# Performance work log

Measured on AMD Instinct MI355X. Metric: run time of the kernel, lower is better.

The kernel has to match this reference:

```python
import jax, jax.numpy as jnp
import numpy as np

B, T, D = 4, 4096, 1024
C = 8.0  # RG_LRU constant c
LOGIT_LO = float(np.log(0.9 / 0.1))    # logit(0.9)
LOGIT_HI = float(np.log(0.999 / 0.001))  # logit(0.999)


def setup_inputs() -> dict:
    key = jax.random.key(0)
    ks = jax.random.split(key, 12)
    s = 1.0 / np.sqrt(D)
    z = lambda: jnp.zeros((D,), jnp.float32)
    return {
        "x": jax.random.normal(ks[0], (B, T, D), jnp.float32),
        "g1": jnp.ones((D,), jnp.float32),
        "g2": jnp.ones((D,), jnp.float32),
        # RecurrentBlock: shared linear, kernel-1 conv, output linear
        "W_lin": jax.random.normal(ks[1], (D, D), jnp.float32) * s, "b_lin": z(),
        "W_conv": jax.random.normal(ks[2], (D, D), jnp.float32) * s, "b_conv": z(),
        "W_lin2": jax.random.normal(ks[3], (D, D), jnp.float32) * s, "b_lin2": z(),
        # RG_LRU params
        "Wa": jax.random.normal(ks[4], (D, D), jnp.float32) * s, "ba": z(),
        "Wx": jax.random.normal(ks[5], (D, D), jnp.float32) * s, "bx": z(),
        "Lam": jax.random.uniform(ks[6], (D,), jnp.float32, LOGIT_LO, LOGIT_HI),
        # GatedMLPBlock
        "W1": jax.random.normal(ks[7], (D, D), jnp.float32) * s, "b1": z(),
        "W2": jax.random.normal(ks[8], (D, D), jnp.float32) * s, "b2": z(),
        "W3": jax.random.normal(ks[9], (D, D), jnp.float32) * s, "b3": z(),
    }


def rms_norm(x, g):
    # F.normalize(x, dim=-1) * sqrt(d) * g
    n = jnp.maximum(jnp.linalg.norm(x, axis=-1, keepdims=True), 1e-12)
    return (x / n) * (x.shape[-1] ** 0.5) * g


def rg_lru(x, Wa, ba, Wx, bx, Lam):
    # x: [B, T, D]
    rt = jax.nn.sigmoid(jnp.einsum('btd,hd->bth', x, Wa) + ba)
    it = jax.nn.sigmoid(jnp.einsum('btd,hd->bth', x, Wx) + bx)
    log_a = -jax.nn.softplus(-Lam)          # [D]
    a = jnp.exp(log_a * rt / C)             # [B, T, D]
    gated = jnp.sqrt(1.0 - a * a) * (it * x)

    def step(h, ag):
        at, gt = ag
        h = at * h + gt
        return h, h

    h0 = jnp.zeros((x.shape[0], x.shape[2]), x.dtype)
    _, hs = jax.lax.scan(step, h0, (jnp.swapaxes(a, 0, 1), jnp.swapaxes(gated, 0, 1)))
    return jnp.swapaxes(hs, 0, 1)           # [B, T, D]


def reference(x, g1, g2, W_lin, b_lin, W_conv, b_conv, W_lin2, b_lin2,
              Wa, ba, Wx, bx, Lam, W1, b1, W2, b2, W3, b3):
    residual = x
    xn = rms_norm(x, g1)

    # RecurrentBlock (note: same linear used for both branches, as in source)
    lin = xn @ W_lin.T + b_lin
    x_gel = jax.nn.gelu(lin, approximate=False)
    x_rg = lin @ W_conv.T + b_conv          # Conv1d kernel_size=1 == pointwise linear
    x_rg = rg_lru(x_rg, Wa, ba, Wx, bx, Lam)
    xr = (x_gel * x_rg) @ W_lin2.T + b_lin2

    residual = xr + residual
    xm = rms_norm(residual, g2)

    # GatedMLPBlock
    out = jax.nn.sigmoid(xm @ W1.T + b1)
    gate = jax.nn.gelu(out, approximate=False)
    combined = gate * (xm @ W2.T + b2)
    y = combined @ W3.T + b3
    return y + residual
```

## Files before the change

kernel.cpp:

```cpp
#include <hip/hip_runtime.h>
#include <cstdint>
#include <cstddef>

typedef unsigned short u16;
typedef __attribute__((ext_vector_type(8))) __bf16 bf16x8;
typedef __attribute__((ext_vector_type(4))) float f32x4;

#define DD 1024
#define MM 16384
#define NCH 64
#define CLEN 64
#define EPAD2 264
#define EPADF 260

__device__ __forceinline__ u16 f2b(float f) {
    uint32_t u = __float_as_uint(f);
    u += 0x7fffu + ((u >> 16) & 1u);
    return (u16)(u >> 16);
}
__device__ __forceinline__ float b2f(u16 v) {
    return __uint_as_float(((uint32_t)v) << 16);
}
__device__ __forceinline__ float sigmoid_f(float v) { return 1.f / (1.f + __expf(-v)); }
__device__ __forceinline__ float gelu_f(float v) {
    return 0.5f * v * (1.f + erff(v * 0.70710678118654752f));
}

__device__ __forceinline__ void glds16(const u16* g, u16* l) {
    __builtin_amdgcn_global_load_lds(
        (const __attribute__((address_space(1))) void*)g,
        (__attribute__((address_space(3))) void*)l, 16, 0, 0);
}

__device__ __forceinline__ void swiz8(int l, int& mt, int& nt) {
    mt = (l & 7) * 8 + ((l >> 3) & 7);
    nt = l >> 6;
}

#define ACC(i, j) ((i) < 4 ? accL[(i) & 3][(j)] : accH[(i) & 3][(j)])

template <int MODE>
__global__ __launch_bounds__(512, 2)
void gemm256(const u16* __restrict__ A, const u16* __restrict__ Bw,
             const float* __restrict__ bias, const float* __restrict__ biasB,
             const float* __restrict__ auxf,
             u16* __restrict__ outb, float* __restrict__ outf)
{
    __shared__ __align__(16) u16 smem[65536];

    int mt, nt; swiz8(blockIdx.x, mt, nt);
    const int m0 = mt * 256, n0 = nt * 256;
    const int tid = threadIdx.x;
    const int wave = tid >> 6, lane = tid & 63;
    const int wm = (wave >> 2) * 128, wn = (wave & 3) * 64;
    const int lr = lane & 15, lq = lane >> 4;

    const int trow = tid >> 2, tcol = tid & 3;
    const int kswz = (tcol ^ ((trow >> 1) & 3)) * 8;
    const u16* Ag = A + (size_t)(m0 + trow) * DD + kswz;
    const u16* Bg = Bw + (size_t)(n0 + trow) * DD + kswz;
    const int st = tid * 8;
    const int cs = (lq ^ ((lr >> 1) & 3)) * 8;

    f32x4 accL[4][4] = {}, accH[4][4] = {};
    bf16x8 av[4], bv[4];

    auto SA = [&](int kt) {
        u16* Ls = smem + (kt & 3) * 16384;
        const u16* a = Ag + (size_t)kt * 32;
        glds16(a, Ls + st);
        glds16(a + (size_t)128 * DD, Ls + 4096 + st);
    };
    auto SB = [&](int kt) {
        u16* Ls = smem + (kt & 3) * 16384 + 8192;
        const u16* b = Bg + (size_t)kt * 32;
        glds16(b, Ls + st);
        glds16(b + (size_t)64 * DD + (size_t)64 * DD, Ls + 4096 + st);
    };
    auto RDA = [&](int kt, int rb) {
        const u16* Ls = smem + (kt & 3) * 16384;
#pragma unroll
        for (int i = 0; i < 4; i++)
            av[i] = *(const bf16x8*)&Ls[(rb + i * 16 + lr) * 32 + cs];
    };
    auto RDB = [&](int kt) {
        const u16* Ls = smem + (kt & 3) * 16384 + 8192;
#pragma unroll
        for (int j = 0; j < 4; j++)
            bv[j] = *(const bf16x8*)&Ls[(wn + j * 16 + lr) * 32 + cs];
    };
    auto MM16 = [&](f32x4 (&ac)[4][4]) {
        __builtin_amdgcn_s_setprio(1);
#pragma unroll
        for (int i = 0; i < 4; i++)
#pragma unroll
            for (int j = 0; j < 4; j++)
                ac[i][j] = __builtin_amdgcn_mfma_f32_16x16x32_bf16(
                    av[i], bv[j], ac[i][j], 0, 0, 0);
        __builtin_amdgcn_s_setprio(0);
    };

    SA(0); SB(0); SA(1); SB(1); SA(2); SB(2);
    asm volatile("s_waitcnt vmcnt(8)\ns_barrier" ::: "memory");

#pragma unroll 4
    for (int kt = 0; kt < 29; ++kt) {
        RDA(kt, wm); RDB(kt);
        SA(kt + 3);
        asm volatile("s_barrier" ::: "memory");
        MM16(accL);
        asm volatile("s_barrier" ::: "memory");
        RDA(kt, wm + 64);
        SB(kt + 3);
        asm volatile("s_waitcnt vmcnt(8)\ns_barrier" ::: "memory");
        MM16(accH);
        asm volatile("s_barrier" ::: "memory");
    }
    RDA(29, wm); RDB(29);
    asm volatile("s_barrier" ::: "memory");
    MM16(accL);
    asm volatile("s_barrier" ::: "memory");
    RDA(29, wm + 64);
    asm volatile("s_waitcnt vmcnt(4)\ns_barrier" ::: "memory");
    MM16(accH);
    asm volatile("s_barrier" ::: "memory");
    RDA(30, wm); RDB(30);
    asm volatile("s_barrier" ::: "memory");
    MM16(accL);
    asm volatile("s_barrier" ::: "memory");
    RDA(30, wm + 64);
    asm volatile("s_waitcnt vmcnt(0)\ns_barrier" ::: "memory");
    MM16(accH);
    asm volatile("s_barrier" ::: "memory");
    RDA(31, wm); RDB(31);
    MM16(accL);
    RDA(31, wm + 64);
    MM16(accH);

    if constexpr (MODE == 0 || MODE == 1) {
        const int NW = (MODE == 1) ? 2048 : 1024;
        u16* ep = smem;
#pragma unroll
        for (int h = 0; h < 4; ++h) {
            __syncthreads();
            if (wm == (h >> 1) * 128) {
                const int i0 = (h & 1) * 4;
#pragma unroll
                for (int ii = 0; ii < 4; ++ii) {
#pragma unroll
                    for (int j = 0; j < 4; ++j) {
                        const int col = wn + j * 16 + lr;
                        const int gc = n0 + col;
                        float bz;
                        if constexpr (MODE == 1)
                            bz = (gc & 1) ? biasB[gc >> 1] : bias[gc >> 1];
                        else
                            bz = bias[gc];
#pragma unroll
                        for (int p = 0; p < 4; ++p) {
                            float v = ACC(i0 + ii, j)[p] + bz;
                            if constexpr (MODE == 1) v = sigmoid_f(v);
                            ep[(ii * 16 + lq * 4 + p) * EPAD2 + col] = f2b(v);
                        }
                    }
                }
            }
            __syncthreads();
#pragma unroll
            for (int t = 0; t < 4; ++t) {
                const int f = t * 512 + tid;
                const int row = f >> 5, c8 = (f & 31) * 8;
                *(uint4*)&outb[(size_t)(m0 + h * 64 + row) * NW + n0 + c8] =
                    *(const uint4*)&ep[row * EPAD2 + c8];
            }
        }
    } else if constexpr (MODE == 2) {
#pragma unroll
        for (int i = 0; i < 8; ++i) {
            const int mrow = m0 + wm + (i & 3) * 16 + (i >> 2) * 64 + lq * 4;
#pragma unroll
            for (int j = 0; j < 4; ++j) {
                const int ncol = n0 + wn + j * 16 + lr;
                const float bz = bias[ncol];
#pragma unroll
                for (int p = 0; p < 4; ++p) {
                    const size_t idx = (size_t)(mrow + p) * DD + ncol;
                    outf[idx] = ((i < 4) ? accL[i & 3][j][p] : accH[i & 3][j][p])
                                + bz + auxf[idx];
                }
            }
        }
    } else {
        float* epf = (float*)smem;
#pragma unroll
        for (int h = 0; h < 4; ++h) {
            __syncthreads();
            if (wm == (h >> 1) * 128) {
                const int i0 = (h & 1) * 4;
#pragma unroll
                for (int ii = 0; ii < 4; ++ii) {
#pragma unroll
                    for (int j = 0; j < 4; ++j) {
                        const int col = wn + j * 16 + lr;
                        const int gc = n0 + col;
                        const float bz = (gc & 1) ? biasB[gc >> 1] : bias[gc >> 1];
#pragma unroll
                        for (int p = 0; p < 4; ++p)
                            epf[(ii * 16 + lq * 4 + p) * EPADF + col] =
                                ACC(i0 + ii, j)[p] + bz;
                    }
                }
            }
            __syncthreads();
#pragma unroll
            for (int t = 0; t < 4; ++t) {
                const int f = t * 512 + tid;
                const int row = f >> 5, cg = (f & 31) * 4;
                const float4 v0 = *(const float4*)&epf[row * EPADF + cg * 2];
                const float4 v1 = *(const float4*)&epf[row * EPADF + cg * 2 + 4];
                ushort4 o4;
                o4.x = f2b(gelu_f(sigmoid_f(v0.x)) * v0.y);
                o4.y = f2b(gelu_f(sigmoid_f(v0.z)) * v0.w);
                o4.z = f2b(gelu_f(sigmoid_f(v1.x)) * v1.y);
                o4.w = f2b(gelu_f(sigmoid_f(v1.z)) * v1.w);
                *(ushort4*)&outb[(size_t)(m0 + h * 64 + row) * DD + (n0 >> 1) + cg] = o4;
            }
        }
    }
}

__global__ __launch_bounds__(256)
void rmsnorm_k(const float* __restrict__ x, const float* __restrict__ g,
               u16* __restrict__ out)
{
    const int row = blockIdx.x;
    const int t = threadIdx.x;
    const float4 v = ((const float4*)(x + (size_t)row * DD))[t];
    float ss = v.x * v.x + v.y * v.y + v.z * v.z + v.w * v.w;
#pragma unroll
    for (int o = 32; o > 0; o >>= 1) ss += __shfl_down(ss, o, 64);
    __shared__ float wsum[4];
    if ((t & 63) == 0) wsum[t >> 6] = ss;
    __syncthreads();
    const float tot = wsum[0] + wsum[1] + wsum[2] + wsum[3];
    const float sc = 32.0f * rsqrtf(fmaxf(tot, 1e-24f));
    const float4 gv = ((const float4*)g)[t];
    ushort4 o4;
    o4.x = f2b(v.x * sc * gv.x);
    o4.y = f2b(v.y * sc * gv.y);
    o4.z = f2b(v.z * sc * gv.z);
    o4.w = f2b(v.w * sc * gv.w);
    ((ushort4*)(out + (size_t)row * DD))[t] = o4;
}

struct WP { const float* s[4]; unsigned off[4]; };
__global__ __launch_bounds__(256)
void conv_plain(WP w, u16* __restrict__ out)
{
    const float* in = w.s[blockIdx.y];
    u16* o = out + (size_t)w.off[blockIdx.y];
    const int i = (blockIdx.x * 256 + threadIdx.x) * 4;
    const float4 v = *(const float4*)(in + i);
    ushort4 r;
    r.x = f2b(v.x); r.y = f2b(v.y); r.z = f2b(v.z); r.w = f2b(v.w);
    *(ushort4*)(o + i) = r;
}
struct WI { const float* a[2]; const float* b[2]; unsigned off[2]; };
__global__ __launch_bounds__(256)
void conv_inter(WI w, u16* __restrict__ out)
{
    u16* o = out + (size_t)w.off[blockIdx.y];
    const int e = (blockIdx.x * 256 + threadIdx.x) * 4;
    const int row = e >> 10, col = e & 1023;
    const float* src = (row & 1) ? w.b[blockIdx.y] : w.a[blockIdx.y];
    const float4 v = *(const float4*)(src + ((size_t)(row >> 1) << 10) + col);
    ushort4 r;
    r.x = f2b(v.x); r.y = f2b(v.y); r.z = f2b(v.z); r.w = f2b(v.w);
    *(ushort4*)(o + e) = r;
}

__global__ __launch_bounds__(256)
void scan_chunks(const u16* __restrict__ rtit, const u16* __restrict__ rg,
                 const float* __restrict__ Lam,
                 float* __restrict__ P, float* __restrict__ Hl)
{
    const int d = blockIdx.x * 256 + threadIdx.x;
    const int c = blockIdx.y, b = blockIdx.z;
    const float k = -log1pf(__expf(-Lam[d])) * 0.125f;
    const size_t base1 = (((size_t)b * 4096) + (size_t)c * CLEN) * DD + d;
    const size_t base2 = (((size_t)b * 4096) + (size_t)c * CLEN) * 2048 + 2 * d;
    float p = 1.f, h = 0.f;
#pragma unroll 4
    for (int t = 0; t < CLEN; t++) {
        const uint32_t w = *(const uint32_t*)&rtit[base2 + (size_t)t * 2048];
        const float r = b2f((u16)(w & 0xffffu));
        const float i = b2f((u16)(w >> 16));
        const float xv = b2f(rg[base1 + (size_t)t * DD]);
        const float a = __expf(k * r);
        const float g = sqrtf(fmaxf(1.f - a * a, 0.f)) * (i * xv);
        p *= a;
        h = fmaf(a, h, g);
    }
    const int o = (b * NCH + c) * DD + d;
    P[o] = p;
    Hl[o] = h;
}

__global__ __launch_bounds__(256)
void scan_carry(const float* __restrict__ P, const float* __restrict__ Hl,
                float* __restrict__ Cin)
{
    const int idx = blockIdx.x * 256 + threadIdx.x;
    const int b = idx >> 10, d = idx & 1023;
    float h = 0.f;
    for (int c = 0; c < NCH; c++) {
        const int o = (b * NCH + c) * DD + d;
        Cin[o] = h;
        h = fmaf(P[o], h, Hl[o]);
    }
}

__global__ __launch_bounds__(256)
void scan_apply(const u16* __restrict__ rtit, const u16* __restrict__ rg,
                const u16* __restrict__ lin, const float* __restrict__ Lam,
                const float* __restrict__ Cin, u16* __restrict__ yin)
{
    const int d = blockIdx.x * 256 + threadIdx.x;
    const int c = blockIdx.y, b = blockIdx.z;
    const float k = -log1pf(__expf(-Lam[d])) * 0.125f;
    const size_t base1 = (((size_t)b * 4096) + (size_t)c * CLEN) * DD + d;
    const size_t base2 = (((size_t)b * 4096) + (size_t)c * CLEN) * 2048 + 2 * d;
    float h = Cin[(b * NCH + c) * DD + d];
#pragma unroll 4
    for (int t = 0; t < CLEN; t++) {
        const uint32_t w = *(const uint32_t*)&rtit[base2 + (size_t)t * 2048];
        const float r = b2f((u16)(w & 0xffffu));
        const float i = b2f((u16)(w >> 16));
        const size_t ix = base1 + (size_t)t * DD;
        const float xv = b2f(rg[ix]);
        const float a = __expf(k * r);
        const float g = sqrtf(fmaxf(1.f - a * a, 0.f)) * (i * xv);
        h = fmaf(a, h, g);
        const float l = b2f(lin[ix]);
        yin[ix] = f2b(gelu_f(l) * h);
    }
}

extern "C" void kernel_launch(void* const* d_in, const int* in_sizes, int n_in,
                              void* d_out, int out_size, void* d_ws, size_t ws_size,
                              hipStream_t stream)
{
    const float* x      = (const float*)d_in[0];
    const float* g1     = (const float*)d_in[1];
    const float* g2     = (const float*)d_in[2];
    const float* W_lin  = (const float*)d_in[3];
    const float* b_lin  = (const float*)d_in[4];
    const float* W_conv = (const float*)d_in[5];
    const float* b_conv = (const float*)d_in[6];
    const float* W_lin2 = (const float*)d_in[7];
    const float* b_lin2 = (const float*)d_in[8];
    const float* Wa     = (const float*)d_in[9];
    const float* ba     = (const float*)d_in[10];
    const float* Wx     = (const float*)d_in[11];
    const float* bx     = (const float*)d_in[12];
    const float* Lam    = (const float*)d_in[13];
    const float* W1     = (const float*)d_in[14];
    const float* b1     = (const float*)d_in[15];
    const float* W2     = (const float*)d_in[16];
    const float* b2     = (const float*)d_in[17];
    const float* W3     = (const float*)d_in[18];
    const float* b3     = (const float*)d_in[19];
    float* out = (float*)d_out;

    char* p = (char*)d_ws;
    auto alloc = [&](size_t bytes) -> char* {
        char* q = p;
        p += (bytes + 255) & ~(size_t)255;
        return q;
    };
    const size_t MD = (size_t)MM * DD;
    const size_t M1 = (size_t)DD * DD;
    u16* wball = (u16*)alloc((size_t)8 * M1 * 2);
    u16* t1   = (u16*)alloc(MD * 2);
    u16* t2   = (u16*)alloc(MD * 2);
    u16* t4   = (u16*)alloc(MD * 2);
    u16* rtit = (u16*)alloc(MD * 4);
    float* res2 = (float*)alloc(MD * 4);
    float* P   = (float*)alloc((size_t)4 * NCH * DD * 4);
    float* Hl  = (float*)alloc((size_t)4 * NCH * DD * 4);
    float* Cin = (float*)alloc((size_t)4 * NCH * DD * 4);

    WP wp;
    wp.s[0] = W_lin;  wp.off[0] = 0;
    wp.s[1] = W_conv; wp.off[1] = 1u << 20;
    wp.s[2] = W_lin2; wp.off[2] = 4u << 20;
    wp.s[3] = W3;     wp.off[3] = 7u << 20;
    conv_plain<<<dim3(M1 / 1024, 4), 256, 0, stream>>>(wp, wball);
    WI wi;
    wi.a[0] = Wa; wi.b[0] = Wx; wi.off[0] = 2u << 20;
    wi.a[1] = W1; wi.b[1] = W2; wi.off[1] = 5u << 20;
    conv_inter<<<dim3(2 * M1 / 1024, 2), 256, 0, stream>>>(wi, wball);

    const u16* wLin  = wball;
    const u16* wConv = wball + (1u << 20);
    const u16* wAX   = wball + (2u << 20);
    const u16* wLin2 = wball + (4u << 20);
    const u16* w12   = wball + (5u << 20);
    const u16* w3    = wball + (7u << 20);

    const int gs = (MM / 256) * (DD / 256);
    const int gw = (MM / 256) * (2 * DD / 256);
    const dim3 sg(DD / 256, NCH, 4);

    rmsnorm_k<<<MM, 256, 0, stream>>>(x, g1, t4);
    gemm256<0><<<gs, 512, 0, stream>>>(t4, wLin, b_lin, nullptr, nullptr, t1, nullptr);
    gemm256<0><<<gs, 512, 0, stream>>>(t1, wConv, b_conv, nullptr, nullptr, t2, nullptr);
    gemm256<1><<<gw, 512, 0, stream>>>(t2, wAX, ba, bx, nullptr, rtit, nullptr);
    scan_chunks<<<sg, 256, 0, stream>>>(rtit, t2, Lam, P, Hl);
    scan_carry<<<4096 / 256, 256, 0, stream>>>(P, Hl, Cin);
    scan_apply<<<sg, 256, 0, stream>>>(rtit, t2, t1, Lam, Cin, t4);
    gemm256<2><<<gs, 512, 0, stream>>>(t4, wLin2, b_lin2, nullptr, x, nullptr, res2);
    rmsnorm_k<<<MM, 256, 0, stream>>>(res2, g2, t4);
    gemm256<3><<<gw, 512, 0, stream>>>(t4, w12, b1, b2, nullptr, t2, nullptr);
    gemm256<2><<<gs, 512, 0, stream>>>(t2, w3, b3, nullptr, res2, nullptr, out);
}
```

Baseline: 605.8 us.

## Use 128x128 tile GEMM kernel for square N=1024 projections

Adds a 256-thread 128x128-tile double-buffered GEMM kernel and routes the four DxD projections (linear, conv, lin2 with residual, W3 with residual) to it, keeping the 256x256 kernel only for the fused N=2048 gate GEMMs. With 256x256 tiles the square GEMMs launch only 256 blocks, which leaves CUs underfilled at 2 blocks per CU. The smaller tile gives 1024 blocks and better occupancy, at the cost of lower operand reuse per tile and a simpler, less pipelined K loop.

```diff
diff --git a/kernel.cpp b/kernel.cpp
--- a/kernel.cpp
+++ b/kernel.cpp
@@ -10,6 +10,7 @@
 #define MM 16384
 #define NCH 64
 #define CLEN 64
+#define EPAD 136
 #define EPAD2 264
 #define EPADF 260
 
@@ -32,9 +33,124 @@
         (__attribute__((address_space(3))) void*)l, 16, 0, 0);
 }
 
+__device__ __forceinline__ void swiz(int l, int& mt, int& nt) {
+    const int g = l >> 6, r = l & 63;
+    mt = g * 8 + (r & 7);
+    nt = r >> 3;
+}
 __device__ __forceinline__ void swiz8(int l, int& mt, int& nt) {
     mt = (l & 7) * 8 + ((l >> 3) & 7);
     nt = l >> 6;
+}
+
+template <int MODE>
+__global__ __launch_bounds__(256, 3)
+void gemm_bt(const u16* __restrict__ A, const u16* __restrict__ Bw,
+             const float* __restrict__ bias, const float* __restrict__ auxf,
+             u16* __restrict__ outb, float* __restrict__ outf)
+{
+    const int K = DD, N = DD;
+    __shared__ __align__(16) u16 smem[16384];
+    u16* const As0 = smem;
+    u16* const Bs0 = smem + 4096;
+    u16* const As1 = smem + 8192;
+    u16* const Bs1 = smem + 12288;
+
+    int mt, nt; swiz(blockIdx.x, mt, nt);
+    const int m0 = mt * 128, n0 = nt * 128;
+    const int tid = threadIdx.x;
+    const int wave = tid >> 6, lane = tid & 63;
+    const int wm = (wave >> 1) * 64, wn = (wave & 1) * 64;
+    const int lr = lane & 15, lq = lane >> 4;
+
+    const int trow = tid >> 2, tcol = tid & 3;
+    const int kswz = (tcol ^ ((trow >> 1) & 3)) * 8;
+    const u16* Ag = A + (size_t)(m0 + trow) * K + kswz;
+    const u16* Bg = Bw + (size_t)(n0 + trow) * K + kswz;
+    const int st = tid * 8;
+    const int cs = (lq ^ ((lr >> 1) & 3)) * 8;
+
+    f32x4 acc[4][4] = {};
+
+    glds16(Ag, As0 + st);
+    glds16(Ag + (size_t)64 * K, As0 + st + 2048);
+    glds16(Bg, Bs0 + st);
+    glds16(Bg + (size_t)64 * K, Bs0 + st + 2048);
+
+#pragma unroll 2
+    for (int k0 = 0; k0 < K; k0 += 32) {
+        u16* const Ac = ((k0 >> 5) & 1) ? As1 : As0;
+        u16* const Bc = ((k0 >> 5) & 1) ? Bs1 : Bs0;
+        if (k0 + 32 < K) {
+            u16* const An = ((k0 >> 5) & 1) ? As0 : As1;
+            u16* const Bn = ((k0 >> 5) & 1) ? Bs0 : Bs1;
+            const int kn = k0 + 32;
+            glds16(Ag + kn, An + st);
+            glds16(Ag + (size_t)64 * K + kn, An + st + 2048);
+            glds16(Bg + kn, Bn + st);
+            glds16(Bg + (size_t)64 * K + kn, Bn + st + 2048);
+            asm volatile("s_waitcnt vmcnt(4)\ns_barrier" ::: "memory");
+        } else {
+            asm volatile("s_waitcnt vmcnt(0)\ns_barrier" ::: "memory");
+        }
+
+        bf16x8 av[4], bv[4];
+#pragma unroll
+        for (int i = 0; i < 4; i++)
+            av[i] = *(const bf16x8*)&Ac[(wm + i * 16 + lr) * 32 + cs];
+#pragma unroll
+        for (int j = 0; j < 4; j++)
+            bv[j] = *(const bf16x8*)&Bc[(wn + j * 16 + lr) * 32 + cs];
+#pragma unroll
+        for (int i = 0; i < 4; i++)
+#pragma unroll
+            for (int j = 0; j < 4; j++)
+                acc[i][j] = __builtin_amdgcn_mfma_f32_16x16x32_bf16(
+                    av[i], bv[j], acc[i][j], 0, 0, 0);
+        asm volatile("s_barrier" ::: "memory");
+    }
+
+    if constexpr (MODE == 0) {
+        for (int half = 0; half < 2; half++) {
+            __syncthreads();
+            if (wm == half * 64) {
+#pragma unroll
+                for (int i = 0; i < 4; i++)
+#pragma unroll
+                    for (int j = 0; j < 4; j++) {
+                        const int col = wn + j * 16 + lr;
+                        const float bz = bias[n0 + col];
+#pragma unroll
+                        for (int p = 0; p < 4; p++)
+                            smem[(i * 16 + lq * 4 + p) * EPAD + col] =
+                                f2b(acc[i][j][p] + bz);
+                    }
+            }
+            __syncthreads();
+#pragma unroll
+            for (int t = 0; t < 4; t++) {
+                const int f = t * 256 + tid;
+                const int row = f >> 4, c8 = (f & 15) * 8;
+                *(uint4*)&outb[(size_t)(m0 + half * 64 + row) * N + n0 + c8] =
+                    *(const uint4*)&smem[row * EPAD + c8];
+            }
+        }
+    } else {
+#pragma unroll
+        for (int i = 0; i < 4; i++) {
+            const int mrow = m0 + wm + i * 16 + lq * 4;
+#pragma unroll
+            for (int j = 0; j < 4; j++) {
+                const int ncol = n0 + wn + j * 16 + lr;
+                const float bz = bias[ncol];
+#pragma unroll
+                for (int p = 0; p < 4; p++) {
+                    const size_t idx = (size_t)(mrow + p) * N + ncol;
+                    outf[idx] = acc[i][j][p] + bz + auxf[idx];
+                }
+            }
+        }
+    }
 }
 
 #define ACC(i, j) ((i) < 4 ? accL[(i) & 3][(j)] : accH[(i) & 3][(j)])
@@ -43,8 +159,7 @@
 __global__ __launch_bounds__(512, 2)
 void gemm256(const u16* __restrict__ A, const u16* __restrict__ Bw,
              const float* __restrict__ bias, const float* __restrict__ biasB,
-             const float* __restrict__ auxf,
-             u16* __restrict__ outb, float* __restrict__ outf)
+             u16* __restrict__ outb)
 {
     __shared__ __align__(16) u16 smem[65536];
 
@@ -75,7 +190,7 @@
         u16* Ls = smem + (kt & 3) * 16384 + 8192;
         const u16* b = Bg + (size_t)kt * 32;
         glds16(b, Ls + st);
-        glds16(b + (size_t)64 * DD + (size_t)64 * DD, Ls + 4096 + st);
+        glds16(b + (size_t)128 * DD, Ls + 4096 + st);
     };
     auto RDA = [&](int kt, int rb) {
         const u16* Ls = smem + (kt & 3) * 16384;
@@ -137,8 +252,7 @@
     RDA(31, wm + 64);
     MM16(accH);
 
-    if constexpr (MODE == 0 || MODE == 1) {
-        const int NW = (MODE == 1) ? 2048 : 1024;
+    if constexpr (MODE == 1) {
         u16* ep = smem;
 #pragma unroll
         for (int h = 0; h < 4; ++h) {
@@ -151,17 +265,11 @@
                     for (int j = 0; j < 4; ++j) {
                         const int col = wn + j * 16 + lr;
                         const int gc = n0 + col;
-                        float bz;
-                        if constexpr (MODE == 1)
-                            bz = (gc & 1) ? biasB[gc >> 1] : bias[gc >> 1];
-                        else
-                            bz = bias[gc];
-#pragma unroll
-                        for (int p = 0; p < 4; ++p) {
-                            float v = ACC(i0 + ii, j)[p] + bz;
-                            if constexpr (MODE == 1) v = sigmoid_f(v);
-                            ep[(ii * 16 + lq * 4 + p) * EPAD2 + col] = f2b(v);
-                        }
+                        const float bz = (gc & 1) ? biasB[gc >> 1] : bias[gc >> 1];
+#pragma unroll
+                        for (int p = 0; p < 4; ++p)
+                            ep[(ii * 16 + lq * 4 + p) * EPAD2 + col] =
+                                f2b(sigmoid_f(ACC(i0 + ii, j)[p] + bz));
                     }
                 }
             }
@@ -170,24 +278,8 @@
             for (int t = 0; t < 4; ++t) {
                 const int f = t * 512 + tid;
                 const int row = f >> 5, c8 = (f & 31) * 8;
-                *(uint4*)&outb[(size_t)(m0 + h * 64 + row) * NW + n0 + c8] =
+                *(uint4*)&outb[(size_t)(m0 + h * 64 + row) * 2048 + n0 + c8] =
                     *(const uint4*)&ep[row * EPAD2 + c8];
-            }
-        }
-    } else if constexpr (MODE == 2) {
-#pragma unroll
-        for (int i = 0; i < 8; ++i) {
-            const int mrow = m0 + wm + (i & 3) * 16 + (i >> 2) * 64 + lq * 4;
-#pragma unroll
-            for (int j = 0; j < 4; ++j) {
-                const int ncol = n0 + wn + j * 16 + lr;
-                const float bz = bias[ncol];
-#pragma unroll
-                for (int p = 0; p < 4; ++p) {
-                    const size_t idx = (size_t)(mrow + p) * DD + ncol;
-                    outf[idx] = ((i < 4) ? accL[i & 3][j][p] : accH[i & 3][j][p])
-                                + bz + auxf[idx];
-                }
             }
         }
     } else {
@@ -408,19 +500,19 @@
     const u16* w12   = wball + (5u << 20);
     const u16* w3    = wball + (7u << 20);
 
-    const int gs = (MM / 256) * (DD / 256);
+    const int gg = (MM / 128) * (DD / 128);
     const int gw = (MM / 256) * (2 * DD / 256);
     const dim3 sg(DD / 256, NCH, 4);
 
     rmsnorm_k<<<MM, 256, 0, stream>>>(x, g1, t4);
-    gemm256<0><<<gs, 512, 0, stream>>>(t4, wLin, b_lin, nullptr, nullptr, t1, nullptr);
-    gemm256<0><<<gs, 512, 0, stream>>>(t1, wConv, b_conv, nullptr, nullptr, t2, nullptr);
-    gemm256<1><<<gw, 512, 0, stream>>>(t2, wAX, ba, bx, nullptr, rtit, nullptr);
+    gemm_bt<0><<<gg, 256, 0, stream>>>(t4, wLin, b_lin, nullptr, t1, nullptr);
+    gemm_bt<0><<<gg, 256, 0, stream>>>(t1, wConv, b_conv, nullptr, t2, nullptr);
+    gemm256<1><<<gw, 512, 0, stream>>>(t2, wAX, ba, bx, rtit);
     scan_chunks<<<sg, 256, 0, stream>>>(rtit, t2, Lam, P, Hl);
     scan_carry<<<4096 / 256, 256, 0, stream>>>(P, Hl, Cin);
     scan_apply<<<sg, 256, 0, stream>>>(rtit, t2, t1, Lam, Cin, t4);
-    gemm256<2><<<gs, 512, 0, stream>>>(t4, wLin2, b_lin2, nullptr, x, nullptr, res2);
+    gemm_bt<2><<<gg, 256, 0, stream>>>(t4, wLin2, b_lin2, x, nullptr, res2);
     rmsnorm_k<<<MM, 256, 0, stream>>>(res2, g2, t4);
-    gemm256<3><<<gw, 512, 0, stream>>>(t4, w12, b1, b2, nullptr, t2, nullptr);
-    gemm256<2><<<gs, 512, 0, stream>>>(t2, w3, b3, nullptr, res2, nullptr, out);
-}
+    gemm256<3><<<gw, 512, 0, stream>>>(t4, w12, b1, b2, t2);
+    gemm_bt<2><<<gg, 256, 0, stream>>>(t2, w3, b3, res2, nullptr, out);
+}
```

Result: slower. 623.4 us (+2.9%).

## Restructure GEMM main loop to K=64 double-buffered tiles with 8-phase schedule

Applied to the files above, without the earlier changes.

Changes the shared GEMM kernel from a 4-stage ring of K=32 tiles to a 2-buffer scheme with K=64 tiles. Global-to-LDS loads are split into half-tile pieces and interleaved across eight MFMA phases per iteration, with a new XOR swizzle sized for 64-wide rows. The aim is to halve loop iterations and barrier overhead per unit of K and to overlap loads with compute more evenly. In exchange, prefetch depth drops to two buffers, which may expose memory latency, and the finer barrier schedule adds synchronization points.

```diff
diff --git a/kernel.cpp b/kernel.cpp
--- a/kernel.cpp
+++ b/kernel.cpp
@@ -38,13 +38,15 @@
 }
 
 #define ACC(i, j) ((i) < 4 ? accL[(i) & 3][(j)] : accH[(i) & 3][(j)])
+#define MFMA16x32(a, b, c) __builtin_amdgcn_mfma_f32_16x16x32_bf16(a, b, c, 0, 0, 0)
+#define BAR asm volatile("s_barrier" ::: "memory")
 
 template <int MODE>
 __global__ __launch_bounds__(512, 2)
-void gemm256(const u16* __restrict__ A, const u16* __restrict__ Bw,
-             const float* __restrict__ bias, const float* __restrict__ biasB,
-             const float* __restrict__ auxf,
-             u16* __restrict__ outb, float* __restrict__ outf)
+void gemm8p(const u16* __restrict__ A, const u16* __restrict__ Bw,
+            const float* __restrict__ bias, const float* __restrict__ biasB,
+            const float* __restrict__ auxf,
+            u16* __restrict__ outb, float* __restrict__ outf)
 {
     __shared__ __align__(16) u16 smem[65536];
 
@@ -55,90 +57,122 @@
     const int wm = (wave >> 2) * 128, wn = (wave & 3) * 64;
     const int lr = lane & 15, lq = lane >> 4;
 
-    const int trow = tid >> 2, tcol = tid & 3;
-    const int kswz = (tcol ^ ((trow >> 1) & 3)) * 8;
-    const u16* Ag = A + (size_t)(m0 + trow) * DD + kswz;
-    const u16* Bg = Bw + (size_t)(n0 + trow) * DD + kswz;
+    const int kswz = ((tid & 7) ^ ((tid >> 3) & 7)) * 8;
+    const u16* Ag = A + (size_t)(m0 + (tid >> 3)) * DD + kswz;
+    const u16* Bg = Bw + (size_t)(n0 + (tid >> 3)) * DD + kswz;
     const int st = tid * 8;
-    const int cs = (lq ^ ((lr >> 1) & 3)) * 8;
+
+    const int cs0 = ((lq ^ (lr & 7))) * 8;
+    const int cs1 = cs0 ^ 32;
+    const int aLo = (wm + lr) * 64;
+    const int bB  = (wn + lr) * 64;
 
     f32x4 accL[4][4] = {}, accH[4][4] = {};
-    bf16x8 av[4], bv[4];
-
-    auto SA = [&](int kt) {
-        u16* Ls = smem + (kt & 3) * 16384;
-        const u16* a = Ag + (size_t)kt * 32;
-        glds16(a, Ls + st);
-        glds16(a + (size_t)128 * DD, Ls + 4096 + st);
-    };
-    auto SB = [&](int kt) {
-        u16* Ls = smem + (kt & 3) * 16384 + 8192;
-        const u16* b = Bg + (size_t)kt * 32;
-        glds16(b, Ls + st);
-        glds16(b + (size_t)64 * DD + (size_t)64 * DD, Ls + 4096 + st);
-    };
-    auto RDA = [&](int kt, int rb) {
-        const u16* Ls = smem + (kt & 3) * 16384;
-#pragma unroll
-        for (int i = 0; i < 4; i++)
-            av[i] = *(const bf16x8*)&Ls[(rb + i * 16 + lr) * 32 + cs];
-    };
-    auto RDB = [&](int kt) {
-        const u16* Ls = smem + (kt & 3) * 16384 + 8192;
-#pragma unroll
-        for (int j = 0; j < 4; j++)
-            bv[j] = *(const bf16x8*)&Ls[(wn + j * 16 + lr) * 32 + cs];
-    };
-    auto MM16 = [&](f32x4 (&ac)[4][4]) {
+    bf16x8 a_lo[4][2], a_hi[4][2], b_lo[2][2], b_hi[2][2];
+
+    auto STA = [&](int kt, int h, int bb) {
+        u16* Ls = smem + bb * 32768 + h * 8192 + st;
+        const u16* g = Ag + (size_t)(h * 128) * DD + kt * 64;
+        glds16(g, Ls);
+        glds16(g + (size_t)64 * DD, Ls + 4096);
+    };
+    auto STB = [&](int kt, int h, int bb) {
+        u16* Ls = smem + bb * 32768 + 16384 + h * 8192 + st;
+        const u16* g = Bg + (size_t)(h * 128) * DD + kt * 64;
+        glds16(g, Ls);
+        glds16(g + (size_t)64 * DD, Ls + 4096);
+    };
+    auto RDA4 = [&](bf16x8 (&a)[4][2], int base) {
+#pragma unroll
+        for (int i = 0; i < 4; i++) {
+            a[i][0] = *(const bf16x8*)&smem[base + i * 1024 + cs0];
+            a[i][1] = *(const bf16x8*)&smem[base + i * 1024 + cs1];
+        }
+    };
+    auto RDB2 = [&](bf16x8 (&b)[2][2], int base) {
+#pragma unroll
+        for (int j = 0; j < 2; j++) {
+            b[j][0] = *(const bf16x8*)&smem[base + j * 1024 + cs0];
+            b[j][1] = *(const bf16x8*)&smem[base + j * 1024 + cs1];
+        }
+    };
+    auto MM_jL = [&](bf16x8 (&a)[4][2], f32x4 (&ac)[4][4]) {
         __builtin_amdgcn_s_setprio(1);
 #pragma unroll
-        for (int i = 0; i < 4; i++)
-#pragma unroll
-            for (int j = 0; j < 4; j++)
-                ac[i][j] = __builtin_amdgcn_mfma_f32_16x16x32_bf16(
-                    av[i], bv[j], ac[i][j], 0, 0, 0);
+        for (int i = 0; i < 4; i++) {
+            ac[i][0] = MFMA16x32(a[i][0], b_lo[0][0], ac[i][0]);
+            ac[i][0] = MFMA16x32(a[i][1], b_lo[0][1], ac[i][0]);
+            ac[i][1] = MFMA16x32(a[i][0], b_lo[1][0], ac[i][1]);
+            ac[i][1] = MFMA16x32(a[i][1], b_lo[1][1], ac[i][1]);
+        }
         __builtin_amdgcn_s_setprio(0);
     };
-
-    SA(0); SB(0); SA(1); SB(1); SA(2); SB(2);
-    asm volatile("s_waitcnt vmcnt(8)\ns_barrier" ::: "memory");
-
-#pragma unroll 4
-    for (int kt = 0; kt < 29; ++kt) {
-        RDA(kt, wm); RDB(kt);
-        SA(kt + 3);
-        asm volatile("s_barrier" ::: "memory");
-        MM16(accL);
-        asm volatile("s_barrier" ::: "memory");
-        RDA(kt, wm + 64);
-        SB(kt + 3);
-        asm volatile("s_waitcnt vmcnt(8)\ns_barrier" ::: "memory");
-        MM16(accH);
-        asm volatile("s_barrier" ::: "memory");
-    }
-    RDA(29, wm); RDB(29);
-    asm volatile("s_barrier" ::: "memory");
-    MM16(accL);
-    asm volatile("s_barrier" ::: "memory");
-    RDA(29, wm + 64);
-    asm volatile("s_waitcnt vmcnt(4)\ns_barrier" ::: "memory");
-    MM16(accH);
-    asm volatile("s_barrier" ::: "memory");
-    RDA(30, wm); RDB(30);
-    asm volatile("s_barrier" ::: "memory");
-    MM16(accL);
-    asm volatile("s_barrier" ::: "memory");
-    RDA(30, wm + 64);
-    asm volatile("s_waitcnt vmcnt(0)\ns_barrier" ::: "memory");
-    MM16(accH);
-    asm volatile("s_barrier" ::: "memory");
-    RDA(31, wm); RDB(31);
-    MM16(accL);
-    RDA(31, wm + 64);
-    MM16(accH);
+    auto MM_jH = [&](bf16x8 (&a)[4][2], f32x4 (&ac)[4][4]) {
+        __builtin_amdgcn_s_setprio(1);
+#pragma unroll
+        for (int i = 0; i < 4; i++) {
+            ac[i][2] = MFMA16x32(a[i][0], b_hi[0][0], ac[i][2]);
+            ac[i][2] = MFMA16x32(a[i][1], b_hi[0][1], ac[i][2]);
+            ac[i][3] = MFMA16x32(a[i][0], b_hi[1][0], ac[i][3]);
+            ac[i][3] = MFMA16x32(a[i][1], b_hi[1][1], ac[i][3]);
+        }
+        __builtin_amdgcn_s_setprio(0);
+    };
+
+    STA(0, 0, 0); STA(0, 1, 0); STB(0, 0, 0); STB(0, 1, 0);
+    STB(1, 0, 1); STB(1, 1, 1); STA(1, 0, 1);
+    asm volatile("s_waitcnt vmcnt(6)\ns_barrier" ::: "memory");
+
+#pragma unroll 2
+    for (int kt = 0; kt < 14; ++kt) {
+        const int db = kt & 1, nb = db ^ 1;
+        const int dbo = db * 32768;
+        RDA4(a_lo, dbo + aLo);
+        RDB2(b_lo, dbo + 16384 + bB);
+        STA(kt + 1, 1, nb);
+        BAR;
+        MM_jL(a_lo, accL);
+        BAR;
+        RDB2(b_hi, dbo + 16384 + bB + 2048);
+        BAR;
+        MM_jH(a_lo, accL);
+        BAR;
+        RDA4(a_hi, dbo + aLo + 4096);
+        STB(kt + 2, 0, db);
+        BAR;
+        MM_jH(a_hi, accH);
+        BAR;
+        STB(kt + 2, 1, db);
+        STA(kt + 2, 0, db);
+        BAR;
+        MM_jL(a_hi, accH);
+        asm volatile("s_waitcnt vmcnt(6)\ns_barrier" ::: "memory");
+    }
+    {
+        RDA4(a_lo, aLo);
+        RDB2(b_lo, 16384 + bB);
+        STA(15, 1, 1);
+        BAR; MM_jL(a_lo, accL); BAR;
+        RDB2(b_hi, 16384 + bB + 2048);
+        BAR; MM_jH(a_lo, accL); BAR;
+        RDA4(a_hi, aLo + 4096);
+        BAR; MM_jH(a_hi, accH); BAR;
+        BAR; MM_jL(a_hi, accH);
+        asm volatile("s_waitcnt vmcnt(0)\ns_barrier" ::: "memory");
+    }
+    {
+        RDA4(a_lo, 32768 + aLo);
+        RDB2(b_lo, 32768 + 16384 + bB);
+        BAR; MM_jL(a_lo, accL); BAR;
+        RDB2(b_hi, 32768 + 16384 + bB + 2048);
+        BAR; MM_jH(a_lo, accL); BAR;
+        RDA4(a_hi, 32768 + aLo + 4096);
+        BAR; MM_jH(a_hi, accH); BAR;
+        BAR; MM_jL(a_hi, accH);
+    }
 
     if constexpr (MODE == 0 || MODE == 1) {
-        const int NW = (MODE == 1) ? 2048 : 1024;
+        constexpr int NW = (MODE == 1) ? 2048 : 1024;
         u16* ep = smem;
 #pragma unroll
         for (int h = 0; h < 4; ++h) {
@@ -413,14 +447,14 @@
     const dim3 sg(DD / 256, NCH, 4);
 
     rmsnorm_k<<<MM, 256, 0, stream>>>(x, g1, t4);
-    gemm256<0><<<gs, 512, 0, stream>>>(t4, wLin, b_lin, nullptr, nullptr, t1, nullptr);
-    gemm256<0><<<gs, 512, 0, stream>>>(t1, wConv, b_conv, nullptr, nullptr, t2, nullptr);
-    gemm256<1><<<gw, 512, 0, stream>>>(t2, wAX, ba, bx, nullptr, rtit, nullptr);
+    gemm8p<0><<<gs, 512, 0, stream>>>(t4, wLin, b_lin, nullptr, nullptr, t1, nullptr);
+    gemm8p<0><<<gs, 512, 0, stream>>>(t1, wConv, b_conv, nullptr, nullptr, t2, nullptr);
+    gemm8p<1><<<gw, 512, 0, stream>>>(t2, wAX, ba, bx, nullptr, rtit, nullptr);
     scan_chunks<<<sg, 256, 0, stream>>>(rtit, t2, Lam, P, Hl);
     scan_carry<<<4096 / 256, 256, 0, stream>>>(P, Hl, Cin);
     scan_apply<<<sg, 256, 0, stream>>>(rtit, t2, t1, Lam, Cin, t4);
-    gemm256<2><<<gs, 512, 0, stream>>>(t4, wLin2, b_lin2, nullptr, x, nullptr, res2);
+    gemm8p<2><<<gs, 512, 0, stream>>>(t4, wLin2, b_lin2, nullptr, x, nullptr, res2);
     rmsnorm_k<<<MM, 256, 0, stream>>>(res2, g2, t4);
-    gemm256<3><<<gw, 512, 0, stream>>>(t4, w12, b1, b2, nullptr, t2, nullptr);
-    gemm256<2><<<gs, 512, 0, stream>>>(t2, w3, b3, nullptr, res2, nullptr, out);
-}
+    gemm8p<3><<<gw, 512, 0, stream>>>(t4, w12, b1, b2, nullptr, t2, nullptr);
+    gemm8p<2><<<gs, 512, 0, stream>>>(t2, w3, b3, nullptr, res2, nullptr, out);
+}
```

Measured after the change: 604.9 us. About the same (-0.1%).

## Restructure GEMM main loop to one barrier per k-step with split A/B LDS buffers

Applied to the files above, without the earlier changes.

Reworks the GEMM's software pipeline. The old loop used four barriers per k-step; the new one waits on vmcnt and barriers once, then issues the A/B prefetch for step t+3 and runs both MFMA halves. LDS is split into separate A and B ring buffers. Fewer barriers should let more MFMA work overlap the global-to-LDS loads. The risk is a race: the prefetch into slot (t+3)&3 could overwrite data other waves are still reading, since the old per-half barriers are gone.

```diff
diff --git a/kernel.cpp b/kernel.cpp
--- a/kernel.cpp
+++ b/kernel.cpp
@@ -38,13 +38,14 @@
 }
 
 #define ACC(i, j) ((i) < 4 ? accL[(i) & 3][(j)] : accH[(i) & 3][(j)])
+#define MFMA16x32(a, b, c) __builtin_amdgcn_mfma_f32_16x16x32_bf16(a, b, c, 0, 0, 0)
 
 template <int MODE>
 __global__ __launch_bounds__(512, 2)
-void gemm256(const u16* __restrict__ A, const u16* __restrict__ Bw,
-             const float* __restrict__ bias, const float* __restrict__ biasB,
-             const float* __restrict__ auxf,
-             u16* __restrict__ outb, float* __restrict__ outf)
+void gemmdp(const u16* __restrict__ A, const u16* __restrict__ Bw,
+            const float* __restrict__ bias, const float* __restrict__ biasB,
+            const float* __restrict__ auxf,
+            u16* __restrict__ outb, float* __restrict__ outf)
 {
     __shared__ __align__(16) u16 smem[65536];
 
@@ -65,80 +66,72 @@
     f32x4 accL[4][4] = {}, accH[4][4] = {};
     bf16x8 av[4], bv[4];
 
-    auto SA = [&](int kt) {
-        u16* Ls = smem + (kt & 3) * 16384;
-        const u16* a = Ag + (size_t)kt * 32;
-        glds16(a, Ls + st);
-        glds16(a + (size_t)128 * DD, Ls + 4096 + st);
-    };
-    auto SB = [&](int kt) {
-        u16* Ls = smem + (kt & 3) * 16384 + 8192;
-        const u16* b = Bg + (size_t)kt * 32;
-        glds16(b, Ls + st);
-        glds16(b + (size_t)64 * DD + (size_t)64 * DD, Ls + 4096 + st);
-    };
-    auto RDA = [&](int kt, int rb) {
-        const u16* Ls = smem + (kt & 3) * 16384;
+    auto STA = [&](int t, int bb) {
+        u16* Ls = smem + bb * 8192 + st;
+        const u16* g = Ag + (size_t)t * 32;
+        glds16(g, Ls);
+        glds16(g + (size_t)128 * DD, Ls + 4096);
+    };
+    auto STB = [&](int t, int bb) {
+        u16* Ls = smem + 32768 + bb * 8192 + st;
+        const u16* g = Bg + (size_t)t * 32;
+        glds16(g, Ls);
+        glds16(g + (size_t)128 * DD, Ls + 4096);
+    };
+    auto RDA = [&](int cb, int off) {
+        const u16* Ls = smem + cb * 8192;
 #pragma unroll
         for (int i = 0; i < 4; i++)
-            av[i] = *(const bf16x8*)&Ls[(rb + i * 16 + lr) * 32 + cs];
-    };
-    auto RDB = [&](int kt) {
-        const u16* Ls = smem + (kt & 3) * 16384 + 8192;
+            av[i] = *(const bf16x8*)&Ls[(wm + off + i * 16 + lr) * 32 + cs];
+    };
+    auto RDB = [&](int cb) {
+        const u16* Ls = smem + 32768 + cb * 8192;
 #pragma unroll
         for (int j = 0; j < 4; j++)
             bv[j] = *(const bf16x8*)&Ls[(wn + j * 16 + lr) * 32 + cs];
     };
-    auto MM16 = [&](f32x4 (&ac)[4][4]) {
+    auto MMP = [&](f32x4 (&ac)[4][4]) {
         __builtin_amdgcn_s_setprio(1);
 #pragma unroll
         for (int i = 0; i < 4; i++)
 #pragma unroll
             for (int j = 0; j < 4; j++)
-                ac[i][j] = __builtin_amdgcn_mfma_f32_16x16x32_bf16(
-                    av[i], bv[j], ac[i][j], 0, 0, 0);
+                ac[i][j] = MFMA16x32(av[i], bv[j], ac[i][j]);
         __builtin_amdgcn_s_setprio(0);
     };
 
-    SA(0); SB(0); SA(1); SB(1); SA(2); SB(2);
+    STA(0, 0); STB(0, 0); STA(1, 1); STB(1, 1); STA(2, 2); STB(2, 2);
+
+    for (int tq = 0; tq < 28; tq += 4) {
+#pragma unroll
+        for (int q = 0; q < 4; ++q) {
+            const int t = tq + q;
+            const int cb = t & 3, sb = (t + 3) & 3;
+            asm volatile("s_waitcnt vmcnt(8)\ns_barrier" ::: "memory");
+            STA(t + 3, sb);
+            RDA(cb, 0); RDB(cb);
+            MMP(accL);
+            STB(t + 3, sb);
+            RDA(cb, 64);
+            MMP(accH);
+        }
+    }
     asm volatile("s_waitcnt vmcnt(8)\ns_barrier" ::: "memory");
-
-#pragma unroll 4
-    for (int kt = 0; kt < 29; ++kt) {
-        RDA(kt, wm); RDB(kt);
-        SA(kt + 3);
-        asm volatile("s_barrier" ::: "memory");
-        MM16(accL);
-        asm volatile("s_barrier" ::: "memory");
-        RDA(kt, wm + 64);
-        SB(kt + 3);
-        asm volatile("s_waitcnt vmcnt(8)\ns_barrier" ::: "memory");
-        MM16(accH);
-        asm volatile("s_barrier" ::: "memory");
-    }
-    RDA(29, wm); RDB(29);
-    asm volatile("s_barrier" ::: "memory");
-    MM16(accL);
-    asm volatile("s_barrier" ::: "memory");
-    RDA(29, wm + 64);
+    STA(31, 3);
+    RDA(0, 0); RDB(0);
+    MMP(accL);
+    STB(31, 3);
+    RDA(0, 64);
+    MMP(accH);
+    asm volatile("s_waitcnt vmcnt(8)\ns_barrier" ::: "memory");
+    RDA(1, 0); RDB(1); MMP(accL); RDA(1, 64); MMP(accH);
     asm volatile("s_waitcnt vmcnt(4)\ns_barrier" ::: "memory");
-    MM16(accH);
-    asm volatile("s_barrier" ::: "memory");
-    RDA(30, wm); RDB(30);
-    asm volatile("s_barrier" ::: "memory");
-    MM16(accL);
-    asm volatile("s_barrier" ::: "memory");
-    RDA(30, wm + 64);
+    RDA(2, 0); RDB(2); MMP(accL); RDA(2, 64); MMP(accH);
     asm volatile("s_waitcnt vmcnt(0)\ns_barrier" ::: "memory");
-    MM16(accH);
-    asm volatile("s_barrier" ::: "memory");
-    RDA(31, wm); RDB(31);
-    MM16(accL);
-    RDA(31, wm + 64);
-    MM16(accH);
+    RDA(3, 0); RDB(3); MMP(accL); RDA(3, 64); MMP(accH);
 
     if constexpr (MODE == 0 || MODE == 1) {
-        const int NW = (MODE == 1) ? 2048 : 1024;
+        constexpr int NW = (MODE == 1) ? 2048 : 1024;
         u16* ep = smem;
 #pragma unroll
         for (int h = 0; h < 4; ++h) {
@@ -413,14 +406,14 @@
     const dim3 sg(DD / 256, NCH, 4);
 
     rmsnorm_k<<<MM, 256, 0, stream>>>(x, g1, t4);
-    gemm256<0><<<gs, 512, 0, stream>>>(t4, wLin, b_lin, nullptr, nullptr, t1, nullptr);
-    gemm256<0><<<gs, 512, 0, stream>>>(t1, wConv, b_conv, nullptr, nullptr, t2, nullptr);
-    gemm256<1><<<gw, 512, 0, stream>>>(t2, wAX, ba, bx, nullptr, rtit, nullptr);
+    gemmdp<0><<<gs, 512, 0, stream>>>(t4, wLin, b_lin, nullptr, nullptr, t1, nullptr);
+    gemmdp<0><<<gs, 512, 0, stream>>>(t1, wConv, b_conv, nullptr, nullptr, t2, nullptr);
+    gemmdp<1><<<gw, 512, 0, stream>>>(t2, wAX, ba, bx, nullptr, rtit, nullptr);
     scan_chunks<<<sg, 256, 0, stream>>>(rtit, t2, Lam, P, Hl);
     scan_carry<<<4096 / 256, 256, 0, stream>>>(P, Hl, Cin);
     scan_apply<<<sg, 256, 0, stream>>>(rtit, t2, t1, Lam, Cin, t4);
-    gemm256<2><<<gs, 512, 0, stream>>>(t4, wLin2, b_lin2, nullptr, x, nullptr, res2);
+    gemmdp<2><<<gs, 512, 0, stream>>>(t4, wLin2, b_lin2, nullptr, x, nullptr, res2);
     rmsnorm_k<<<MM, 256, 0, stream>>>(res2, g2, t4);
-    gemm256<3><<<gw, 512, 0, stream>>>(t4, w12, b1, b2, nullptr, t2, nullptr);
-    gemm256<2><<<gs, 512, 0, stream>>>(t2, w3, b3, nullptr, res2, nullptr, out);
-}
+    gemmdp<3><<<gw, 512, 0, stream>>>(t4, w12, b1, b2, nullptr, t2, nullptr);
+    gemmdp<2><<<gs, 512, 0, stream>>>(t2, w3, b3, nullptr, res2, nullptr, out);
+}
```

Result: slower. 620.5 us (+2.4%).
